# Optimization experiments

Measured on AMD Instinct MI355X. Metric: run time of the kernel, lower is better.

Reference implementation:

```python
import jax, jax.numpy as jnp
import numpy as np

D_MODEL = 1024
EXPERT_DIM = 2048
N_EXPERTS = 8
LN_EPS = 1e-5


def _bit_quant(W):
    # W: [out, in] (or [..., out, in]); per-output-row ternary quantization with STE
    scale = jnp.clip(jnp.mean(jnp.abs(W), axis=-1, keepdims=True), 1e-5, None)
    w_q = jnp.clip(jnp.round(W / scale), -1.0, 1.0) * scale
    return W + jax.lax.stop_gradient(w_q - W)


def setup_inputs() -> dict:
    key = jax.random.key(0)
    ks = jax.random.split(key, 7)
    x = jax.random.normal(ks[0], (4, 2048, D_MODEL), dtype=jnp.float32)
    # kaiming_normal fan_out, linear -> std = 1/sqrt(out_features)
    shared_w1 = jax.random.normal(ks[1], (EXPERT_DIM, D_MODEL), dtype=jnp.float32) / np.sqrt(EXPERT_DIM)
    shared_w2 = jax.random.normal(ks[2], (D_MODEL, EXPERT_DIM), dtype=jnp.float32) / np.sqrt(D_MODEL)
    expert_w1 = jax.random.normal(ks[3], (N_EXPERTS, EXPERT_DIM, D_MODEL), dtype=jnp.float32) / np.sqrt(EXPERT_DIM)
    expert_w2 = jax.random.normal(ks[4], (N_EXPERTS, D_MODEL, EXPERT_DIM), dtype=jnp.float32) / np.sqrt(D_MODEL)
    router_w = 0.02 * jax.random.normal(ks[5], (N_EXPERTS, D_MODEL), dtype=jnp.float32)
    ln_gamma = jnp.ones((D_MODEL,), dtype=jnp.float32)
    ln_beta = jnp.zeros((D_MODEL,), dtype=jnp.float32)
    return {"x": x, "shared_w1": shared_w1, "shared_w2": shared_w2,
            "expert_w1": expert_w1, "expert_w2": expert_w2,
            "router_w": router_w, "ln_gamma": ln_gamma, "ln_beta": ln_beta}


def reference(x, shared_w1, shared_w2, expert_w1, expert_w2, router_w, ln_gamma, ln_beta):
    # LayerNorm
    mu = jnp.mean(x, axis=-1, keepdims=True)
    var = jnp.mean(jnp.square(x - mu), axis=-1, keepdims=True)
    h = (x - mu) / jnp.sqrt(var + LN_EPS) * ln_gamma + ln_beta  # [B,T,D]

    # Shared expert (BitLinear -> SiLU -> BitLinear)
    sw1, sw2 = _bit_quant(shared_w1), _bit_quant(shared_w2)
    shared_out = jax.nn.silu(jnp.einsum('btd,fd->btf', h, sw1)) @ sw2.T  # [B,T,D]

    # Top-1 router
    probs = jax.nn.softmax(h @ router_w.T, axis=-1)  # [B,T,E]
    top_prob = jnp.max(probs, axis=-1)               # [B,T]
    top_idx = jnp.argmax(probs, axis=-1)             # [B,T]

    # Routed experts: compute all experts densely, select via one-hot gate
    ew1, ew2 = _bit_quant(expert_w1), _bit_quant(expert_w2)
    h1 = jax.nn.silu(jnp.einsum('btd,efd->ebtf', h, ew1))      # [E,B,T,F]
    eo = jnp.einsum('ebtf,edf->ebtd', h1, ew2)                 # [E,B,T,D]
    gate = jax.nn.one_hot(top_idx, N_EXPERTS, dtype=h.dtype) * top_prob[..., None]  # [B,T,E]
    routed_out = jnp.einsum('ebtd,bte->btd', eo, gate)

    return shared_out + routed_out
```

## Files before the change

### kernel.cpp

```cpp
#include <hip/hip_runtime.h>
#include <hip/hip_bf16.h>

#define D_MODEL 1024
#define F_DIM   2048
#define NE      8
#define NTOK    8192
#define MAXT    72
#define HBLK    32

typedef __attribute__((ext_vector_type(8))) short bf16x8;
typedef __attribute__((ext_vector_type(4))) float f32x4;

__device__ __forceinline__ unsigned short f2b(float f) {
    unsigned int u = __float_as_uint(f);
    u += 0x7FFFu + ((u >> 16) & 1u);
    return (unsigned short)(u >> 16);
}
__device__ __forceinline__ unsigned int pack2(float a, float b) {
    return (unsigned int)f2b(a) | ((unsigned int)f2b(b) << 16);
}
__device__ __forceinline__ void async16(const void* g, void* l) {
    __builtin_amdgcn_global_load_lds((const __attribute__((address_space(1))) void*)g,
                                     (__attribute__((address_space(3))) void*)l, 16, 0, 0);
}

template <int K>
__global__ __launch_bounds__(256) void quant_rows(const float* __restrict__ W,
                                                  unsigned short* __restrict__ Q) {
    constexpr int PER = K / 256;
    constexpr int PV  = PER / 4;
    __shared__ float sred[4];
    const int tid = threadIdx.x;
    const size_t row = blockIdx.x;
    const float4* Wv = (const float4*)(W + row * (size_t)K) + tid * PV;
    float4 v[PV];
#pragma unroll
    for (int i = 0; i < PV; i++) v[i] = Wv[i];
    float s = 0.f;
#pragma unroll
    for (int i = 0; i < PV; i++)
        s += fabsf(v[i].x) + fabsf(v[i].y) + fabsf(v[i].z) + fabsf(v[i].w);
#pragma unroll
    for (int o = 32; o > 0; o >>= 1) s += __shfl_down(s, o);
    if ((tid & 63) == 0) sred[tid >> 6] = s;
    __syncthreads();
    float scale = (sred[0] + sred[1] + sred[2] + sred[3]) * (1.0f / K);
    scale = fmaxf(scale, 1e-5f);
    const float inv = 1.0f / scale;
    unsigned int* Qu = (unsigned int*)(Q + row * (size_t)K) + tid * (PER / 2);
#pragma unroll
    for (int i = 0; i < PV; i++) {
        float q0 = fminf(1.f, fmaxf(-1.f, rintf(v[i].x * inv))) * scale;
        float q1 = fminf(1.f, fmaxf(-1.f, rintf(v[i].y * inv))) * scale;
        float q2 = fminf(1.f, fmaxf(-1.f, rintf(v[i].z * inv))) * scale;
        float q3 = fminf(1.f, fmaxf(-1.f, rintf(v[i].w * inv))) * scale;
        Qu[2 * i]     = pack2(q0, q1);
        Qu[2 * i + 1] = pack2(q2, q3);
    }
}

__global__ __launch_bounds__(256) void ln_router(const float* __restrict__ x,
                                                 const float* __restrict__ gamma,
                                                 const float* __restrict__ beta,
                                                 const float* __restrict__ rw,
                                                 unsigned short* __restrict__ h,
                                                 int* __restrict__ top_idx,
                                                 float* __restrict__ top_prob) {
    const int lane = threadIdx.x & 63;
    const size_t tok = blockIdx.x * 4 + (threadIdx.x >> 6);

    const float4* xr = (const float4*)(x + tok * D_MODEL);
    float4 xv[4];
#pragma unroll
    for (int i = 0; i < 4; i++) xv[i] = xr[lane + 64 * i];
    float s = 0.f, q = 0.f;
#pragma unroll
    for (int i = 0; i < 4; i++) {
        s += xv[i].x + xv[i].y + xv[i].z + xv[i].w;
        q += xv[i].x * xv[i].x + xv[i].y * xv[i].y + xv[i].z * xv[i].z + xv[i].w * xv[i].w;
    }
#pragma unroll
    for (int o = 32; o > 0; o >>= 1) { s += __shfl_down(s, o); q += __shfl_down(q, o); }
    s = __shfl(s, 0); q = __shfl(q, 0);
    const float mean = s * (1.0f / D_MODEL);
    const float rstd = rsqrtf(q * (1.0f / D_MODEL) - mean * mean + 1e-5f);

    float4 hv[4];
    unsigned int* hr = (unsigned int*)(h + tok * D_MODEL);
#pragma unroll
    for (int i = 0; i < 4; i++) {
        const float4 g  = ((const float4*)gamma)[lane + 64 * i];
        const float4 bt = ((const float4*)beta)[lane + 64 * i];
        hv[i].x = (xv[i].x - mean) * rstd * g.x + bt.x;
        hv[i].y = (xv[i].y - mean) * rstd * g.y + bt.y;
        hv[i].z = (xv[i].z - mean) * rstd * g.z + bt.z;
        hv[i].w = (xv[i].w - mean) * rstd * g.w + bt.w;
        hr[2 * (lane + 64 * i)]     = pack2(hv[i].x, hv[i].y);
        hr[2 * (lane + 64 * i) + 1] = pack2(hv[i].z, hv[i].w);
    }

    float acc[NE];
#pragma unroll
    for (int e = 0; e < NE; e++) {
        const float4* rr = (const float4*)(rw + e * D_MODEL);
        float a = 0.f;
#pragma unroll
        for (int i = 0; i < 4; i++) {
            const float4 r = rr[lane + 64 * i];
            a += hv[i].x * r.x + hv[i].y * r.y + hv[i].z * r.z + hv[i].w * r.w;
        }
        acc[e] = a;
    }
#pragma unroll
    for (int e = 0; e < NE; e++) {
#pragma unroll
        for (int o = 32; o > 0; o >>= 1) acc[e] += __shfl_down(acc[e], o);
    }
    if (lane == 0) {
        float m = acc[0]; int bi = 0;
#pragma unroll
        for (int e = 1; e < NE; e++) { if (acc[e] > m) { m = acc[e]; bi = e; } }
        float se = 0.f;
#pragma unroll
        for (int e = 0; e < NE; e++) se += __expf(acc[e] - m);
        top_idx[tok]  = bi;
        top_prob[tok] = 1.0f / se;
    }
}

__global__ __launch_bounds__(256) void hist_kernel(const int* __restrict__ top_idx,
                                                   int* __restrict__ blockhist) {
    __shared__ int lh[NE];
    if (threadIdx.x < NE) lh[threadIdx.x] = 0;
    __syncthreads();
    const int t = blockIdx.x * 256 + threadIdx.x;
    atomicAdd(&lh[top_idx[t]], 1);
    __syncthreads();
    if (threadIdx.x < NE) blockhist[blockIdx.x * NE + threadIdx.x] = lh[threadIdx.x];
}

__global__ __launch_bounds__(256) void scan_plan(const int* __restrict__ blockhist,
                                                 int* __restrict__ base,
                                                 int4* __restrict__ tilemap,
                                                 int* __restrict__ tok_perm) {
    __shared__ int sh[HBLK * NE];
    __shared__ int counts[NE];
    __shared__ int offsets[NE];
    __shared__ int tstart[NE + 1];
    const int tid = threadIdx.x;
    sh[tid] = blockhist[tid];
    __syncthreads();
    if (tid < NE) {
        int c = 0;
#pragma unroll
        for (int b = 0; b < HBLK; b++) c += sh[b * NE + tid];
        counts[tid] = c;
    }
    __syncthreads();
    if (tid == 0) {
        int off = 0, slot = 0;
#pragma unroll
        for (int e = 0; e < NE; e++) {
            offsets[e] = off;
            tstart[e] = slot;
            slot += (counts[e] + 127) >> 7;
            off += counts[e];
        }
        tstart[NE] = slot;
    }
    __syncthreads();
    if (tid < MAXT) {
        int4 t; t.x = 0; t.y = 0; t.z = 0; t.w = 0;
#pragma unroll
        for (int e = 0; e < NE; e++) {
            if (tid >= tstart[e] && tid < tstart[e + 1]) {
                const int k = (tid - tstart[e]) << 7;
                t.x = e; t.y = offsets[e] + k; t.z = min(128, counts[e] - k);
            }
        }
        tilemap[tid] = t;
    }
    {
        const int b = tid >> 3, e = tid & 7;
        int r = offsets[e];
        for (int bb = 0; bb < b; bb++) r += sh[bb * NE + e];
        base[b * NE + e] = r;
    }
    if (tid < 128) tok_perm[NTOK + tid] = 0;
}

__global__ __launch_bounds__(256) void scatter_tokens(const int* __restrict__ top_idx,
                                                      const float* __restrict__ top_prob,
                                                      const int* __restrict__ base,
                                                      int* __restrict__ tok_perm,
                                                      float* __restrict__ probg) {
    __shared__ int cur[NE];
    if (threadIdx.x < NE) cur[threadIdx.x] = base[blockIdx.x * NE + threadIdx.x];
    __syncthreads();
    const int t = blockIdx.x * 256 + threadIdx.x;
    const int e = top_idx[t];
    const int pos = atomicAdd(&cur[e], 1);
    tok_perm[pos] = t;
    probg[pos] = top_prob[t];
}

template <int MODE>
__global__ __launch_bounds__(256) void gemm64(const unsigned short* __restrict__ A,
                                              const unsigned short* __restrict__ Bmain,
                                              const unsigned short* __restrict__ Bexp,
                                              unsigned short* __restrict__ C1s,
                                              unsigned short* __restrict__ C1r,
                                              float* __restrict__ Out,
                                              int N, int K,
                                              const int4* __restrict__ tilemap,
                                              const int* __restrict__ tok_perm,
                                              const float* __restrict__ probg) {
    constexpr unsigned GX = (MODE == 0) ? (F_DIM / 128) : (D_MODEL / 128);
    const unsigned flat = blockIdx.y * GX + blockIdx.x;
    const unsigned nwg  = gridDim.y * GX;
    const unsigned swz  = (flat & 7u) * (nwg >> 3) + (flat >> 3);
    const unsigned bx   = swz & (GX - 1u);
    const unsigned by   = swz / GX;

    int m0, rowsValid;
    const unsigned short* B;
    unsigned short* Cb = nullptr;
    bool gather = false;
    if (MODE == 0) {
        if (by < 64) {
            m0 = by * 128; rowsValid = 128; B = Bmain; Cb = C1s;
        } else {
            int4 tm = tilemap[by - 64];
            if (tm.z == 0) return;
            m0 = tm.y; rowsValid = tm.z;
            B = Bexp + (size_t)tm.x * F_DIM * D_MODEL;
            Cb = C1r; gather = true;
        }
    } else if (MODE == 1) {
        int4 tm = tilemap[by];
        if (tm.z == 0) return;
        m0 = tm.y; rowsValid = tm.z;
        B = Bmain + (size_t)tm.x * D_MODEL * F_DIM;
    } else {
        m0 = by * 128; rowsValid = 128; B = Bmain;
    }
    const int n0 = bx * 128;

    __shared__ unsigned short As[128 * 64];
    __shared__ unsigned short Bs[128 * 64];

    const int tid = threadIdx.x;
    const int lane = tid & 63;
    const int w = tid >> 6;
    const int wm = w >> 1, wn = w & 1;

    f32x4 acc[4][4];
#pragma unroll
    for (int i = 0; i < 4; i++)
#pragma unroll
        for (int j = 0; j < 4; j++) acc[i][j] = (f32x4){0.f, 0.f, 0.f, 0.f};

    const int sRow = lane >> 3;
    const int sCol = ((lane & 7) ^ sRow) * 8;
    const unsigned short* aP[4];
    const unsigned short* bP[4];
#pragma unroll
    for (int qq = 0; qq < 4; qq++) {
        const int ra = w * 32 + qq * 8 + sRow;
        size_t arow;
        if (MODE == 0) arow = gather ? (size_t)tok_perm[m0 + ra] : (size_t)(m0 + ra);
        else           arow = (size_t)(m0 + ra);
        aP[qq] = A + arow * (size_t)K + sCol;
        bP[qq] = B + (size_t)(n0 + ra) * K + sCol;
    }
    unsigned short* aL = As + w * 2048;
    unsigned short* bL = Bs + w * 2048;

    const int fr = lane & 15, fq = lane >> 4;
    const bf16x8* Ar = (const bf16x8*)As;
    const bf16x8* Br = (const bf16x8*)Bs;

    for (int k0 = 0; k0 < K; k0 += 64) {
#pragma unroll
        for (int qq = 0; qq < 4; qq++) async16(aP[qq] + k0, aL + qq * 512);
#pragma unroll
        for (int qq = 0; qq < 4; qq++) async16(bP[qq] + k0, bL + qq * 512);
        __syncthreads();
#pragma unroll
        for (int kc = 0; kc < 2; kc++) {
            bf16x8 af[4], bfr[4];
#pragma unroll
            for (int i = 0; i < 4; i++) {
                const int row = wm * 64 + i * 16 + fr;
                af[i] = Ar[row * 8 + (((kc << 2) + fq) ^ (fr & 7))];
            }
#pragma unroll
            for (int j = 0; j < 4; j++) {
                const int row = wn * 64 + j * 16 + fr;
                bfr[j] = Br[row * 8 + (((kc << 2) + fq) ^ (fr & 7))];
            }
#pragma unroll
            for (int i = 0; i < 4; i++)
#pragma unroll
                for (int j = 0; j < 4; j++)
                    acc[i][j] = __builtin_amdgcn_mfma_f32_16x16x32_bf16(af[i], bfr[j], acc[i][j], 0, 0, 0);
        }
        __syncthreads();
    }

#pragma unroll
    for (int i = 0; i < 4; i++) {
        const int rb = wm * 64 + i * 16 + fq * 4;
#pragma unroll
        for (int t = 0; t < 4; t++) {
            const int r = rb + t;
            if (r < rowsValid) {
#pragma unroll
                for (int j = 0; j < 4; j++) {
                    const int c = n0 + wn * 64 + j * 16 + fr;
                    float v = acc[i][j][t];
                    if (MODE == 0) {
                        const float den = 1.0f + __expf(-v);
                        v = v * __builtin_amdgcn_rcpf(den);
                        Cb[(size_t)(m0 + r) * N + c] = f2b(v);
                    } else if (MODE == 1) {
                        const int tokr = tok_perm[m0 + r];
                        Out[(size_t)tokr * N + c] = probg[m0 + r] * v;
                    } else {
                        float* o = Out + (size_t)(m0 + r) * N + c;
                        *o = *o + v;
                    }
                }
            }
        }
    }
}

extern "C" void kernel_launch(void* const* d_in, const int* in_sizes, int n_in,
                              void* d_out, int out_size, void* d_ws, size_t ws_size,
                              hipStream_t stream) {
    const float* x   = (const float*)d_in[0];
    const float* sw1 = (const float*)d_in[1];
    const float* sw2 = (const float*)d_in[2];
    const float* ew1 = (const float*)d_in[3];
    const float* ew2 = (const float*)d_in[4];
    const float* rw  = (const float*)d_in[5];
    const float* gam = (const float*)d_in[6];
    const float* bet = (const float*)d_in[7];
    float* out = (float*)d_out;

    char* ws = (char*)d_ws;
    const size_t H_OFF    = 0;
    const size_t SW1Q_OFF = H_OFF + (size_t)NTOK * D_MODEL * 2;
    const size_t SW2Q_OFF = SW1Q_OFF + (size_t)F_DIM * D_MODEL * 2;
    const size_t EW1Q_OFF = SW2Q_OFF + (size_t)D_MODEL * F_DIM * 2;
    const size_t EW2Q_OFF = EW1Q_OFF + (size_t)NE * F_DIM * D_MODEL * 2;
    const size_t H1S_OFF  = EW2Q_OFF + (size_t)NE * D_MODEL * F_DIM * 2;
    const size_t H1R_OFF  = H1S_OFF + (size_t)NTOK * F_DIM * 2;
    const size_t PERM_OFF = H1R_OFF + (size_t)(NTOK + 128) * F_DIM * 2;
    const size_t PROBG_OFF = PERM_OFF + (NTOK + 128) * 4;
    const size_t IDX_OFF   = PROBG_OFF + NTOK * 4;
    const size_t PROB_OFF  = IDX_OFF + NTOK * 4;
    const size_t BH_OFF    = PROB_OFF + NTOK * 4;
    const size_t BASE_OFF  = BH_OFF + HBLK * NE * 4;
    const size_t TILE_OFF  = BASE_OFF + HBLK * NE * 4;

    unsigned short* h     = (unsigned short*)(ws + H_OFF);
    unsigned short* sw1q  = (unsigned short*)(ws + SW1Q_OFF);
    unsigned short* sw2q  = (unsigned short*)(ws + SW2Q_OFF);
    unsigned short* ew1q  = (unsigned short*)(ws + EW1Q_OFF);
    unsigned short* ew2q  = (unsigned short*)(ws + EW2Q_OFF);
    unsigned short* h1s   = (unsigned short*)(ws + H1S_OFF);
    unsigned short* h1r   = (unsigned short*)(ws + H1R_OFF);
    int*   tok_perm = (int*)(ws + PERM_OFF);
    float* probg    = (float*)(ws + PROBG_OFF);
    int*   idx      = (int*)(ws + IDX_OFF);
    float* prob     = (float*)(ws + PROB_OFF);
    int*   blockhist = (int*)(ws + BH_OFF);
    int*   base      = (int*)(ws + BASE_OFF);
    int4*  tilemap   = (int4*)(ws + TILE_OFF);

    quant_rows<1024><<<2048, 256, 0, stream>>>(sw1, sw1q);
    quant_rows<2048><<<1024, 256, 0, stream>>>(sw2, sw2q);
    quant_rows<1024><<<16384, 256, 0, stream>>>(ew1, ew1q);
    quant_rows<2048><<<8192, 256, 0, stream>>>(ew2, ew2q);

    ln_router<<<NTOK / 4, 256, 0, stream>>>(x, gam, bet, rw, h, idx, prob);

    hist_kernel<<<HBLK, 256, 0, stream>>>(idx, blockhist);
    scan_plan<<<1, 256, 0, stream>>>(blockhist, base, tilemap, tok_perm);
    scatter_tokens<<<HBLK, 256, 0, stream>>>(idx, prob, base, tok_perm, probg);

    gemm64<0><<<dim3(F_DIM / 128, 64 + MAXT), 256, 0, stream>>>(
        h, sw1q, ew1q, h1s, h1r, nullptr, F_DIM, D_MODEL, tilemap, tok_perm, nullptr);

    gemm64<1><<<dim3(D_MODEL / 128, MAXT), 256, 0, stream>>>(
        h1r, ew2q, nullptr, nullptr, nullptr, out, D_MODEL, F_DIM, tilemap, tok_perm, probg);
    gemm64<2><<<dim3(D_MODEL / 128, NTOK / 128), 256, 0, stream>>>(
        h1s, sw2q, nullptr, nullptr, nullptr, out, D_MODEL, F_DIM, tilemap, tok_perm, probg);
}
```

Measured before the change: 425.8 us.

## Fuse weight quantization with LayerNorm and merge routed and shared second GEMMs

All four weight-quantization kernels and the LayerNorm/router kernel now run as one launch that dispatches on block index. The second-stage routed-expert GEMM and the shared-expert down-projection are merged into one kernel. Each tile first accumulates the expert product, scales it by the router probability, then keeps accumulating the shared product for the same permuted tokens and writes the output once. This removes the read-modify-write of the output in fp32 and several launches, at the cost of gathered A-row loads for the shared pass and relying on the tilemap padding to cover all tokens.

```diff
diff --git a/kernel.cpp b/kernel.cpp
--- a/kernel.cpp
+++ b/kernel.cpp
@@ -25,14 +25,13 @@
 }
 
 template <int K>
-__global__ __launch_bounds__(256) void quant_rows(const float* __restrict__ W,
-                                                  unsigned short* __restrict__ Q) {
+__device__ __forceinline__ void quant_dev(const float* __restrict__ W,
+                                          unsigned short* __restrict__ Q,
+                                          int row, float* sred) {
     constexpr int PER = K / 256;
     constexpr int PV  = PER / 4;
-    __shared__ float sred[4];
     const int tid = threadIdx.x;
-    const size_t row = blockIdx.x;
-    const float4* Wv = (const float4*)(W + row * (size_t)K) + tid * PV;
+    const float4* Wv = (const float4*)(W + (size_t)row * K) + tid * PV;
     float4 v[PV];
 #pragma unroll
     for (int i = 0; i < PV; i++) v[i] = Wv[i];
@@ -47,7 +46,7 @@
     float scale = (sred[0] + sred[1] + sred[2] + sred[3]) * (1.0f / K);
     scale = fmaxf(scale, 1e-5f);
     const float inv = 1.0f / scale;
-    unsigned int* Qu = (unsigned int*)(Q + row * (size_t)K) + tid * (PER / 2);
+    unsigned int* Qu = (unsigned int*)(Q + (size_t)row * K) + tid * (PER / 2);
 #pragma unroll
     for (int i = 0; i < PV; i++) {
         float q0 = fminf(1.f, fmaxf(-1.f, rintf(v[i].x * inv))) * scale;
@@ -59,15 +58,16 @@
     }
 }
 
-__global__ __launch_bounds__(256) void ln_router(const float* __restrict__ x,
-                                                 const float* __restrict__ gamma,
-                                                 const float* __restrict__ beta,
-                                                 const float* __restrict__ rw,
-                                                 unsigned short* __restrict__ h,
-                                                 int* __restrict__ top_idx,
-                                                 float* __restrict__ top_prob) {
+__device__ __forceinline__ void ln_dev(const float* __restrict__ x,
+                                       const float* __restrict__ gamma,
+                                       const float* __restrict__ beta,
+                                       const float* __restrict__ rw,
+                                       unsigned short* __restrict__ h,
+                                       int* __restrict__ top_idx,
+                                       float* __restrict__ top_prob,
+                                       int blk) {
     const int lane = threadIdx.x & 63;
-    const size_t tok = blockIdx.x * 4 + (threadIdx.x >> 6);
+    const size_t tok = (size_t)blk * 4 + (threadIdx.x >> 6);
 
     const float4* xr = (const float4*)(x + tok * D_MODEL);
     float4 xv[4];
@@ -126,6 +126,30 @@
         top_idx[tok]  = bi;
         top_prob[tok] = 1.0f / se;
     }
+}
+
+__global__ __launch_bounds__(256) void fused_pre(const float* __restrict__ sw1,
+                                                 const float* __restrict__ sw2,
+                                                 const float* __restrict__ ew1,
+                                                 const float* __restrict__ ew2,
+                                                 unsigned short* __restrict__ sw1q,
+                                                 unsigned short* __restrict__ sw2q,
+                                                 unsigned short* __restrict__ ew1q,
+                                                 unsigned short* __restrict__ ew2q,
+                                                 const float* __restrict__ x,
+                                                 const float* __restrict__ gamma,
+                                                 const float* __restrict__ beta,
+                                                 const float* __restrict__ rw,
+                                                 unsigned short* __restrict__ h,
+                                                 int* __restrict__ top_idx,
+                                                 float* __restrict__ top_prob) {
+    __shared__ float sred[4];
+    const int b = blockIdx.x;
+    if (b < 2048)       quant_dev<1024>(sw1, sw1q, b, sred);
+    else if (b < 3072)  quant_dev<2048>(sw2, sw2q, b - 2048, sred);
+    else if (b < 19456) quant_dev<1024>(ew1, ew1q, b - 3072, sred);
+    else if (b < 27648) quant_dev<2048>(ew2, ew2q, b - 19456, sred);
+    else                ln_dev(x, gamma, beta, rw, h, top_idx, top_prob, b - 27648);
 }
 
 __global__ __launch_bounds__(256) void hist_kernel(const int* __restrict__ top_idx,
@@ -204,18 +228,15 @@
     probg[pos] = top_prob[t];
 }
 
-template <int MODE>
-__global__ __launch_bounds__(256) void gemm64(const unsigned short* __restrict__ A,
-                                              const unsigned short* __restrict__ Bmain,
-                                              const unsigned short* __restrict__ Bexp,
-                                              unsigned short* __restrict__ C1s,
-                                              unsigned short* __restrict__ C1r,
-                                              float* __restrict__ Out,
-                                              int N, int K,
-                                              const int4* __restrict__ tilemap,
-                                              const int* __restrict__ tok_perm,
-                                              const float* __restrict__ probg) {
-    constexpr unsigned GX = (MODE == 0) ? (F_DIM / 128) : (D_MODEL / 128);
+__global__ __launch_bounds__(256) void gemm_g1(const unsigned short* __restrict__ A,
+                                               const unsigned short* __restrict__ Bmain,
+                                               const unsigned short* __restrict__ Bexp,
+                                               unsigned short* __restrict__ C1s,
+                                               unsigned short* __restrict__ C1r,
+                                               const int4* __restrict__ tilemap,
+                                               const int* __restrict__ tok_perm) {
+    constexpr int N = F_DIM, K = D_MODEL;
+    constexpr unsigned GX = F_DIM / 128;
     const unsigned flat = blockIdx.y * GX + blockIdx.x;
     const unsigned nwg  = gridDim.y * GX;
     const unsigned swz  = (flat & 7u) * (nwg >> 3) + (flat >> 3);
@@ -224,25 +245,16 @@
 
     int m0, rowsValid;
     const unsigned short* B;
-    unsigned short* Cb = nullptr;
+    unsigned short* Cb;
     bool gather = false;
-    if (MODE == 0) {
-        if (by < 64) {
-            m0 = by * 128; rowsValid = 128; B = Bmain; Cb = C1s;
-        } else {
-            int4 tm = tilemap[by - 64];
-            if (tm.z == 0) return;
-            m0 = tm.y; rowsValid = tm.z;
-            B = Bexp + (size_t)tm.x * F_DIM * D_MODEL;
-            Cb = C1r; gather = true;
-        }
-    } else if (MODE == 1) {
-        int4 tm = tilemap[by];
+    if (by < 64) {
+        m0 = by * 128; rowsValid = 128; B = Bmain; Cb = C1s;
+    } else {
+        int4 tm = tilemap[by - 64];
         if (tm.z == 0) return;
         m0 = tm.y; rowsValid = tm.z;
-        B = Bmain + (size_t)tm.x * D_MODEL * F_DIM;
-    } else {
-        m0 = by * 128; rowsValid = 128; B = Bmain;
+        B = Bexp + (size_t)tm.x * F_DIM * D_MODEL;
+        Cb = C1r; gather = true;
     }
     const int n0 = bx * 128;
 
@@ -267,9 +279,7 @@
 #pragma unroll
     for (int qq = 0; qq < 4; qq++) {
         const int ra = w * 32 + qq * 8 + sRow;
-        size_t arow;
-        if (MODE == 0) arow = gather ? (size_t)tok_perm[m0 + ra] : (size_t)(m0 + ra);
-        else           arow = (size_t)(m0 + ra);
+        size_t arow = gather ? (size_t)tok_perm[m0 + ra] : (size_t)(m0 + ra);
         aP[qq] = A + arow * (size_t)K + sCol;
         bP[qq] = B + (size_t)(n0 + ra) * K + sCol;
     }
@@ -319,17 +329,133 @@
                 for (int j = 0; j < 4; j++) {
                     const int c = n0 + wn * 64 + j * 16 + fr;
                     float v = acc[i][j][t];
-                    if (MODE == 0) {
-                        const float den = 1.0f + __expf(-v);
-                        v = v * __builtin_amdgcn_rcpf(den);
-                        Cb[(size_t)(m0 + r) * N + c] = f2b(v);
-                    } else if (MODE == 1) {
-                        const int tokr = tok_perm[m0 + r];
-                        Out[(size_t)tokr * N + c] = probg[m0 + r] * v;
-                    } else {
-                        float* o = Out + (size_t)(m0 + r) * N + c;
-                        *o = *o + v;
-                    }
+                    const float den = 1.0f + __expf(-v);
+                    v = v * __builtin_amdgcn_rcpf(den);
+                    Cb[(size_t)(m0 + r) * N + c] = f2b(v);
+                }
+            }
+        }
+    }
+}
+
+__global__ __launch_bounds__(256) void gemm_g2(const unsigned short* __restrict__ A1,
+                                               const unsigned short* __restrict__ A2,
+                                               const unsigned short* __restrict__ Bexp,
+                                               const unsigned short* __restrict__ Bsh,
+                                               float* __restrict__ Out,
+                                               const int4* __restrict__ tilemap,
+                                               const int* __restrict__ tok_perm,
+                                               const float* __restrict__ probg) {
+    constexpr int N = D_MODEL, K = F_DIM;
+    constexpr unsigned GX = D_MODEL / 128;
+    const unsigned flat = blockIdx.y * GX + blockIdx.x;
+    const unsigned nwg  = gridDim.y * GX;
+    const unsigned swz  = (flat & 7u) * (nwg >> 3) + (flat >> 3);
+    const unsigned bx   = swz & (GX - 1u);
+    const unsigned by   = swz / GX;
+
+    int4 tm = tilemap[by];
+    if (tm.z == 0) return;
+    const int m0 = tm.y, rowsValid = tm.z;
+    const unsigned short* B1 = Bexp + (size_t)tm.x * D_MODEL * F_DIM;
+    const int n0 = bx * 128;
+
+    __shared__ unsigned short As[128 * 64];
+    __shared__ unsigned short Bs[128 * 64];
+
+    const int tid = threadIdx.x;
+    const int lane = tid & 63;
+    const int w = tid >> 6;
+    const int wm = w >> 1, wn = w & 1;
+    const int fr = lane & 15, fq = lane >> 4;
+
+    f32x4 acc[4][4];
+#pragma unroll
+    for (int i = 0; i < 4; i++)
+#pragma unroll
+        for (int j = 0; j < 4; j++) acc[i][j] = (f32x4){0.f, 0.f, 0.f, 0.f};
+
+    float ps[4][4];
+#pragma unroll
+    for (int i = 0; i < 4; i++)
+#pragma unroll
+        for (int t = 0; t < 4; t++)
+            ps[i][t] = probg[m0 + wm * 64 + i * 16 + fq * 4 + t];
+
+    const int sRow = lane >> 3;
+    const int sCol = ((lane & 7) ^ sRow) * 8;
+    unsigned short* aL = As + w * 2048;
+    unsigned short* bL = Bs + w * 2048;
+    const bf16x8* Ar = (const bf16x8*)As;
+    const bf16x8* Br = (const bf16x8*)Bs;
+
+    const unsigned short* aP[4];
+    const unsigned short* bP[4];
+
+#pragma unroll
+    for (int qq = 0; qq < 4; qq++) {
+        const int ra = w * 32 + qq * 8 + sRow;
+        aP[qq] = A1 + (size_t)(m0 + ra) * K + sCol;
+        bP[qq] = B1 + (size_t)(n0 + ra) * K + sCol;
+    }
+
+#pragma unroll 1
+    for (int pass = 0; pass < 2; pass++) {
+        for (int k0 = 0; k0 < K; k0 += 64) {
+#pragma unroll
+            for (int qq = 0; qq < 4; qq++) async16(aP[qq] + k0, aL + qq * 512);
+#pragma unroll
+            for (int qq = 0; qq < 4; qq++) async16(bP[qq] + k0, bL + qq * 512);
+            __syncthreads();
+#pragma unroll
+            for (int kc = 0; kc < 2; kc++) {
+                bf16x8 af[4], bfr[4];
+#pragma unroll
+                for (int i = 0; i < 4; i++) {
+                    const int row = wm * 64 + i * 16 + fr;
+                    af[i] = Ar[row * 8 + (((kc << 2) + fq) ^ (fr & 7))];
+                }
+#pragma unroll
+                for (int j = 0; j < 4; j++) {
+                    const int row = wn * 64 + j * 16 + fr;
+                    bfr[j] = Br[row * 8 + (((kc << 2) + fq) ^ (fr & 7))];
+                }
+#pragma unroll
+                for (int i = 0; i < 4; i++)
+#pragma unroll
+                    for (int j = 0; j < 4; j++)
+                        acc[i][j] = __builtin_amdgcn_mfma_f32_16x16x32_bf16(af[i], bfr[j], acc[i][j], 0, 0, 0);
+            }
+            __syncthreads();
+        }
+        if (pass == 0) {
+#pragma unroll
+            for (int i = 0; i < 4; i++)
+#pragma unroll
+                for (int j = 0; j < 4; j++)
+#pragma unroll
+                    for (int t = 0; t < 4; t++) acc[i][j][t] *= ps[i][t];
+#pragma unroll
+            for (int qq = 0; qq < 4; qq++) {
+                const int ra = w * 32 + qq * 8 + sRow;
+                aP[qq] = A2 + (size_t)tok_perm[m0 + ra] * K + sCol;
+                bP[qq] = Bsh + (size_t)(n0 + ra) * K + sCol;
+            }
+        }
+    }
+
+#pragma unroll
+    for (int i = 0; i < 4; i++) {
+        const int rb = wm * 64 + i * 16 + fq * 4;
+#pragma unroll
+        for (int t = 0; t < 4; t++) {
+            const int r = rb + t;
+            if (r < rowsValid) {
+                const int tokr = tok_perm[m0 + r];
+#pragma unroll
+                for (int j = 0; j < 4; j++) {
+                    const int c = n0 + wn * 64 + j * 16 + fr;
+                    Out[(size_t)tokr * N + c] = acc[i][j][t];
                 }
             }
         }
@@ -359,7 +485,7 @@
     const size_t H1R_OFF  = H1S_OFF + (size_t)NTOK * F_DIM * 2;
     const size_t PERM_OFF = H1R_OFF + (size_t)(NTOK + 128) * F_DIM * 2;
     const size_t PROBG_OFF = PERM_OFF + (NTOK + 128) * 4;
-    const size_t IDX_OFF   = PROBG_OFF + NTOK * 4;
+    const size_t IDX_OFF   = PROBG_OFF + (NTOK + 128) * 4;
     const size_t PROB_OFF  = IDX_OFF + NTOK * 4;
     const size_t BH_OFF    = PROB_OFF + NTOK * 4;
     const size_t BASE_OFF  = BH_OFF + HBLK * NE * 4;
@@ -380,22 +506,16 @@
     int*   base      = (int*)(ws + BASE_OFF);
     int4*  tilemap   = (int4*)(ws + TILE_OFF);
 
-    quant_rows<1024><<<2048, 256, 0, stream>>>(sw1, sw1q);
-    quant_rows<2048><<<1024, 256, 0, stream>>>(sw2, sw2q);
-    quant_rows<1024><<<16384, 256, 0, stream>>>(ew1, ew1q);
-    quant_rows<2048><<<8192, 256, 0, stream>>>(ew2, ew2q);
-
-    ln_router<<<NTOK / 4, 256, 0, stream>>>(x, gam, bet, rw, h, idx, prob);
+    fused_pre<<<29696, 256, 0, stream>>>(sw1, sw2, ew1, ew2, sw1q, sw2q, ew1q, ew2q,
+                                         x, gam, bet, rw, h, idx, prob);
 
     hist_kernel<<<HBLK, 256, 0, stream>>>(idx, blockhist);
     scan_plan<<<1, 256, 0, stream>>>(blockhist, base, tilemap, tok_perm);
     scatter_tokens<<<HBLK, 256, 0, stream>>>(idx, prob, base, tok_perm, probg);
 
-    gemm64<0><<<dim3(F_DIM / 128, 64 + MAXT), 256, 0, stream>>>(
-        h, sw1q, ew1q, h1s, h1r, nullptr, F_DIM, D_MODEL, tilemap, tok_perm, nullptr);
-
-    gemm64<1><<<dim3(D_MODEL / 128, MAXT), 256, 0, stream>>>(
-        h1r, ew2q, nullptr, nullptr, nullptr, out, D_MODEL, F_DIM, tilemap, tok_perm, probg);
-    gemm64<2><<<dim3(D_MODEL / 128, NTOK / 128), 256, 0, stream>>>(
-        h1s, sw2q, nullptr, nullptr, nullptr, out, D_MODEL, F_DIM, tilemap, tok_perm, probg);
-}
+    gemm_g1<<<dim3(F_DIM / 128, 64 + MAXT), 256, 0, stream>>>(
+        h, sw1q, ew1q, h1s, h1r, tilemap, tok_perm);
+
+    gemm_g2<<<dim3(D_MODEL / 128, MAXT), 256, 0, stream>>>(
+        h1r, h1s, ew2q, sw2q, out, tilemap, tok_perm, probg);
+}
```

Measured after the change: 445.9 us. 1.05x slower.
